# Optimization experiments

Measured on AMD Instinct MI355X. Metric: run time of the kernel, lower is better.

## Reference

```python
import jax, jax.numpy as jnp
import numpy as np
import math

STATE_SIZE = 32


def setup_inputs() -> dict:
    key = jax.random.key(0)
    k1, k2, k3, k4, k5 = jax.random.split(key, 5)
    B, C, H, W = 8, STATE_SIZE, 512, 512
    std = 1.0 / math.sqrt(C)
    states = jax.random.normal(k1, (B, C, H, W), dtype=jnp.float32)
    weight_ih = jax.random.uniform(k2, (3 * C, 3 * C), minval=-std, maxval=std, dtype=jnp.float32)
    bias_ih = jax.random.uniform(k3, (3 * C,), minval=-std, maxval=std, dtype=jnp.float32)
    weight_hh = jax.random.uniform(k4, (3 * C, C), minval=-std, maxval=std, dtype=jnp.float32)
    bias_hh = jax.random.uniform(k5, (3 * C,), minval=-std, maxval=std, dtype=jnp.float32)
    return {"states": states, "weight_ih": weight_ih, "bias_ih": bias_ih,
            "weight_hh": weight_hh, "bias_hh": bias_hh}


def _cell(prev_col, cur_col, weight_ih, bias_ih, weight_hh, bias_hh):
    # prev_col, cur_col: (B, H, C)
    C = cur_col.shape[-1]
    pad = jnp.pad(prev_col, ((0, 0), (1, 1), (0, 0)))  # zero-pad H
    # 3-neighbor gather along H: rows h-1, h, h+1 of previous column
    x = jnp.concatenate([pad[:, :-2], pad[:, 1:-1], pad[:, 2:]], axis=-1)  # (B, H, 3C)
    i_vals = jnp.einsum('bhk,ok->bho', x, weight_ih) + bias_ih            # (B, H, 3C)
    h_vals = jnp.einsum('bhc,oc->bho', cur_col, weight_hh) + bias_hh      # (B, H, 3C)
    r_i, z_i, n_i = jnp.split(i_vals, 3, axis=-1)
    r_h, z_h, n_h = jnp.split(h_vals, 3, axis=-1)
    r = jax.nn.sigmoid(r_i + r_h)
    z = jax.nn.sigmoid(z_i + z_h)
    n = jnp.tanh(n_i + r * n_h)
    return n * z + cur_col * (1.0 - z)


def reference(states, weight_ih, bias_ih, weight_hh, bias_hh):
    # states: (B, C, H, W); scan over W (dir=0, left-to-right)
    s = jnp.transpose(states, (3, 0, 2, 1))  # (W, B, H, C)

    def step(carry, cur_col):
        new_col = _cell(carry, cur_col, weight_ih, bias_ih, weight_hh, bias_hh)
        return new_col, new_col

    col0 = s[0]
    _, cols = jax.lax.scan(step, col0, s[1:])
    out = jnp.concatenate([col0[None], cols], axis=0)  # (W, B, H, C)
    return jnp.transpose(out, (1, 3, 2, 0))  # (B, C, H, W)
```

## Files before the change

kernel.cpp:

```cpp
#include <hip/hip_runtime.h>
#include <stdint.h>
#include <stddef.h>

typedef __attribute__((ext_vector_type(8))) short short8;
typedef __attribute__((ext_vector_type(4))) float floatx4;
typedef unsigned long long u64;

#define Bn 8
#define Cn 32
#define Hn 512
#define Wn 512
#define NCH 32
#define RR 16
#define GR 8
#define WT 8
#define NT (Wn/WT)
#define NWG (Bn*NCH)
#define PST 40
#define OST 9

__device__ __forceinline__ unsigned short f2bf(float f) {
  union { float f; unsigned int i; } v; v.f = f;
  unsigned int x = v.i;
  unsigned int r = x + 0x7fffu + ((x >> 16) & 1u);
  return (unsigned short)(r >> 16);
}
__device__ __forceinline__ float sigmoidf_(float x) {
  return 1.0f / (1.0f + __expf(-x));
}
__device__ __forceinline__ float tanhf_(float x) {
  return 1.0f - 2.0f / (__expf(2.0f * x) + 1.0f);
}

__global__ __launch_bounds__(256, 1) void sdn_scan(
    const float* __restrict__ states,
    const float* __restrict__ wih,
    const float* __restrict__ bih,
    const float* __restrict__ whh,
    const float* __restrict__ bhh,
    float* __restrict__ out,
    u64* __restrict__ bnd)
{
  const int tid = threadIdx.x;
  const int lane = tid & 63;
  const int wid = tid >> 6;
  const int tl = wid >> 1;
  const int tt = wid & 1;
  const int wg = blockIdx.x;
  const int b = wg & 7;
  const int j = wg >> 3;
  const int h0 = j * RR;
  const int lm = lane & 15;
  const int lg = lane >> 4;
  const int cS = lane >> 1;
  const int qS = lane & 1;

  __shared__ __align__(16) unsigned short P[34 * PST];
  __shared__ __align__(16) float INS[WT * 32 * 32];
  __shared__ __align__(16) float OUTS[RR * 32 * OST];

  short8 wf[3][3];
  short8 hf[3];
  float bi[3], bh[3];
  for (int q = 0; q < 3; ++q) {
    const int ot = 2 * q + tt;
    for (int ks = 0; ks < 3; ++ks) {
      short8 v;
#pragma unroll
      for (int t = 0; t < 8; ++t)
        v[t] = (short)f2bf(wih[(size_t)(16 * ot + lm) * 96 + 32 * ks + lg * 8 + t]);
      wf[q][ks] = v;
    }
    short8 v;
#pragma unroll
    for (int t = 0; t < 8; ++t)
      v[t] = (short)f2bf(whh[(size_t)(16 * ot + lm) * 32 + lg * 8 + t]);
    hf[q] = v;
    bi[q] = bih[16 * ot + lm];
    bh[q] = bhh[16 * ot + lm];
  }

  auto stage = [&](int w0) {
    float4 buf[8];
#pragma unroll
    for (int r = 0; r < 8; ++r) {
      int row = 8 * wid + r;
      int h = h0 - GR + row;
      buf[r].x = 0.f; buf[r].y = 0.f; buf[r].z = 0.f; buf[r].w = 0.f;
      if ((unsigned)h < (unsigned)Hn)
        buf[r] = *(const float4*)&states[(((size_t)b * Cn + cS) * Hn + h) * Wn + w0 + 4 * qS];
    }
#pragma unroll
    for (int r = 0; r < 8; ++r) {
      int row = 8 * wid + r;
      float* dst = &INS[row * 32 + cS];
      dst[(4 * qS + 0) * 1024] = buf[r].x;
      dst[(4 * qS + 1) * 1024] = buf[r].y;
      dst[(4 * qS + 2) * 1024] = buf[r].z;
      dst[(4 * qS + 3) * 1024] = buf[r].w;
    }
  };

  stage(0);
  __syncthreads();
  for (int t = tid; t < 34 * 32; t += 256) {
    int pr = t >> 5, c = t & 31;
    int rr = pr - 1;
    unsigned short v = 0;
    if ((unsigned)rr < 32u) v = f2bf(INS[rr * 32 + c]);
    P[pr * PST + c] = v;
  }
  for (int t = tid; t < RR * 32; t += 256) {
    int r = t >> 5, c = t & 31;
    OUTS[(r * 32 + c) * OST + 0] = INS[(r + 8) * 32 + c];
  }
  __syncthreads();

  for (int t = 0; t < NT; ++t) {
    const int w0 = WT * t;

    for (int wi = (t == 0) ? 1 : 0; wi < WT; ++wi) {
      const float* INw = &INS[wi * 1024];

      short8 af[3];
#pragma unroll
      for (int ks = 0; ks < 3; ++ks)
        af[ks] = *(const short8*)&P[(16 * tl + lm + ks) * PST + lg * 8];

      short8 curA;
      {
        const float* ap = &INw[(16 * tl + lm) * 32 + 8 * lg];
#pragma unroll
        for (int u = 0; u < 8; ++u) curA[u] = (short)f2bf(ap[u]);
      }
      float curC[4];
#pragma unroll
      for (int i = 0; i < 4; ++i)
        curC[i] = INw[(16 * tl + 4 * lg + i) * 32 + 16 * tt + lm];

      __syncthreads();

      floatx4 I[3], Hh[3];
#pragma unroll
      for (int q = 0; q < 3; ++q) {
        I[q] = (floatx4){bi[q], bi[q], bi[q], bi[q]};
        Hh[q] = (floatx4){bh[q], bh[q], bh[q], bh[q]};
#pragma unroll
        for (int ks = 0; ks < 3; ++ks)
          I[q] = __builtin_amdgcn_mfma_f32_16x16x32_bf16(af[ks], wf[q][ks], I[q], 0, 0, 0);
        Hh[q] = __builtin_amdgcn_mfma_f32_16x16x32_bf16(curA, hf[q], Hh[q], 0, 0, 0);
      }
#pragma unroll
      for (int i = 0; i < 4; ++i) {
        float rv = sigmoidf_(I[0][i] + Hh[0][i]);
        float zv = sigmoidf_(I[1][i] + Hh[1][i]);
        float nv = tanhf_(I[2][i] + rv * Hh[2][i]);
        float ov = curC[i] + zv * (nv - curC[i]);
        int c = 16 * tt + lm;
        int rr = 16 * tl + 4 * lg + i;
        unsigned short pv = f2bf(ov);
        if ((j == 0 && rr == 7) || (j == NCH - 1 && rr == 24)) pv = 0;
        P[(1 + rr) * PST + c] = pv;
        bool own = (tl == 0) ? (lg >= 2) : (lg < 2);
        if (own)
          OUTS[((rr - 8) * 32 + c) * OST + wi] = ov;
      }

      __syncthreads();
    }

    const int par = t & 1;
    const unsigned int tag = (unsigned int)(w0 + 7);

    if (t < NT - 1) {
      const int dir = tid >> 7;
      const int idx = tid & 127;
      const int row = idx >> 4, cp = (idx & 15) * 2;
      const int prow = (dir ? 17 : 9) + row;
      u64 v = (u64)((unsigned int)P[prow * PST + cp] |
                    ((unsigned int)P[prow * PST + cp + 1] << 16)) | ((u64)tag << 32);
      __hip_atomic_store(&bnd[(size_t)(wg * 2 + par) * 256 + tid], v,
                         __ATOMIC_RELAXED, __HIP_MEMORY_SCOPE_AGENT);
    }

#pragma unroll
    for (int r4 = 0; r4 < 4; ++r4) {
      int r = 4 * wid + r4;
      const float* src = &OUTS[(r * 32 + cS) * OST + 4 * qS];
      float4 v;
      v.x = src[0]; v.y = src[1]; v.z = src[2]; v.w = src[3];
      *(float4*)&out[(((size_t)b * Cn + cS) * Hn + (h0 + r)) * Wn + w0 + 4 * qS] = v;
    }

    if (t < NT - 1) {
      stage(w0 + WT);

      if (tid < 128) {
        if (j > 0) {
          const u64* src = &bnd[(size_t)((wg - 8) * 2 + par) * 256 + 128 + tid];
          u64 v; int spins = 0;
          while (true) {
            v = __hip_atomic_load(src, __ATOMIC_RELAXED, __HIP_MEMORY_SCOPE_AGENT);
            if ((unsigned int)(v >> 32) == tag) break;
            __builtin_amdgcn_s_sleep(2);
            if (++spins > (1 << 20)) break;
          }
          int row = tid >> 4, cp = (tid & 15) * 2;
          P[(1 + row) * PST + cp] = (unsigned short)(v & 0xffffu);
          P[(1 + row) * PST + cp + 1] = (unsigned short)((v >> 16) & 0xffffu);
        }
      } else {
        if (j < NCH - 1) {
          const int idx = tid - 128;
          const u64* src = &bnd[(size_t)((wg + 8) * 2 + par) * 256 + idx];
          u64 v; int spins = 0;
          while (true) {
            v = __hip_atomic_load(src, __ATOMIC_RELAXED, __HIP_MEMORY_SCOPE_AGENT);
            if ((unsigned int)(v >> 32) == tag) break;
            __builtin_amdgcn_s_sleep(2);
            if (++spins > (1 << 20)) break;
          }
          int row = idx >> 4, cp = (idx & 15) * 2;
          P[(25 + row) * PST + cp] = (unsigned short)(v & 0xffffu);
          P[(25 + row) * PST + cp + 1] = (unsigned short)((v >> 16) & 0xffffu);
        }
      }

      __syncthreads();
    }
  }
}

extern "C" void kernel_launch(void* const* d_in, const int* in_sizes, int n_in,
                              void* d_out, int out_size, void* d_ws, size_t ws_size,
                              hipStream_t stream) {
  const float* states = (const float*)d_in[0];
  const float* wih = (const float*)d_in[1];
  const float* bih = (const float*)d_in[2];
  const float* whh = (const float*)d_in[3];
  const float* bhh = (const float*)d_in[4];
  float* outp = (float*)d_out;

  u64* bnd = (u64*)d_ws;

  hipMemsetAsync(bnd, 0, (size_t)NWG * 2 * 256 * sizeof(u64), stream);

  sdn_scan<<<dim3(NWG), dim3(256), 0, stream>>>(states, wih, bih, whh, bhh, outp, bnd);
}
```

Measured before the change: 968.0 us.

## Double-buffer prev column, prefetch next tile, pre-convert bf16 inputs, keep outputs in registers

Double-buffers the bf16 previous-column array so each column step needs one barrier instead of two. The next tile of global input is loaded into registers before the column loop so its latency overlaps compute. Inputs are converted to bf16 once at staging time and the next column's operands are prefetched ahead. Outputs stay in registers and are written straight to global memory, dropping the OUTS shared buffer. In exchange it uses more registers, and the buffer parity logic depends on the tile width being even.

```diff
diff --git a/kernel.cpp b/kernel.cpp
--- a/kernel.cpp
+++ b/kernel.cpp
@@ -17,7 +17,8 @@
 #define NT (Wn/WT)
 #define NWG (Bn*NCH)
 #define PST 40
-#define OST 9
+#define IST 40
+#define IPL (32*IST)
 
 __device__ __forceinline__ unsigned short f2bf(float f) {
   union { float f; unsigned int i; } v; v.f = f;
@@ -55,9 +56,9 @@
   const int cS = lane >> 1;
   const int qS = lane & 1;
 
-  __shared__ __align__(16) unsigned short P[34 * PST];
+  __shared__ __align__(16) unsigned short Pb[2][34 * PST];
   __shared__ __align__(16) float INS[WT * 32 * 32];
-  __shared__ __align__(16) float OUTS[RR * 32 * OST];
+  __shared__ __align__(16) unsigned short INB[WT * IPL];
 
   short8 wf[3][3];
   short8 hf[3];
@@ -80,7 +81,7 @@
     bh[q] = bhh[16 * ot + lm];
   }
 
-  auto stage = [&](int w0) {
+  {
     float4 buf[8];
 #pragma unroll
     for (int r = 0; r < 8; ++r) {
@@ -88,85 +89,119 @@
       int h = h0 - GR + row;
       buf[r].x = 0.f; buf[r].y = 0.f; buf[r].z = 0.f; buf[r].w = 0.f;
       if ((unsigned)h < (unsigned)Hn)
-        buf[r] = *(const float4*)&states[(((size_t)b * Cn + cS) * Hn + h) * Wn + w0 + 4 * qS];
+        buf[r] = *(const float4*)&states[(((size_t)b * Cn + cS) * Hn + h) * Wn + 4 * qS];
     }
 #pragma unroll
     for (int r = 0; r < 8; ++r) {
       int row = 8 * wid + r;
       float* dst = &INS[row * 32 + cS];
-      dst[(4 * qS + 0) * 1024] = buf[r].x;
-      dst[(4 * qS + 1) * 1024] = buf[r].y;
-      dst[(4 * qS + 2) * 1024] = buf[r].z;
-      dst[(4 * qS + 3) * 1024] = buf[r].w;
-    }
-  };
-
-  stage(0);
+      unsigned short* bdst = &INB[row * IST + cS];
+      dst[(4 * qS + 0) * 1024] = buf[r].x;  bdst[(4 * qS + 0) * IPL] = f2bf(buf[r].x);
+      dst[(4 * qS + 1) * 1024] = buf[r].y;  bdst[(4 * qS + 1) * IPL] = f2bf(buf[r].y);
+      dst[(4 * qS + 2) * 1024] = buf[r].z;  bdst[(4 * qS + 2) * IPL] = f2bf(buf[r].z);
+      dst[(4 * qS + 3) * 1024] = buf[r].w;  bdst[(4 * qS + 3) * IPL] = f2bf(buf[r].w);
+    }
+  }
   __syncthreads();
+
   for (int t = tid; t < 34 * 32; t += 256) {
     int pr = t >> 5, c = t & 31;
     int rr = pr - 1;
     unsigned short v = 0;
     if ((unsigned)rr < 32u) v = f2bf(INS[rr * 32 + c]);
-    P[pr * PST + c] = v;
-  }
-  for (int t = tid; t < RR * 32; t += 256) {
-    int r = t >> 5, c = t & 31;
-    OUTS[(r * 32 + c) * OST + 0] = INS[(r + 8) * 32 + c];
+    Pb[0][pr * PST + c] = v;
+  }
+  if (tid < 64) {
+    int pr = (tid >= 32) ? 33 : 0, c = tid & 31;
+    Pb[1][pr * PST + c] = 0;
   }
   __syncthreads();
+
+  float oreg[4][8];
+  {
+    const int c = 16 * tt + lm;
+#pragma unroll
+    for (int i = 0; i < 4; ++i)
+      oreg[i][0] = INS[(16 * tl + 4 * lg + i) * 32 + c];
+  }
+
+  int cur = 0;
 
   for (int t = 0; t < NT; ++t) {
     const int w0 = WT * t;
 
-    for (int wi = (t == 0) ? 1 : 0; wi < WT; ++wi) {
-      const float* INw = &INS[wi * 1024];
+    float4 sbuf[8];
+    if (t < NT - 1) {
+#pragma unroll
+      for (int r = 0; r < 8; ++r) {
+        int row = 8 * wid + r;
+        int h = h0 - GR + row;
+        sbuf[r].x = 0.f; sbuf[r].y = 0.f; sbuf[r].z = 0.f; sbuf[r].w = 0.f;
+        if ((unsigned)h < (unsigned)Hn)
+          sbuf[r] = *(const float4*)&states[(((size_t)b * Cn + cS) * Hn + h) * Wn + (w0 + WT) + 4 * qS];
+      }
+    }
+
+    const int wf0 = (t == 0) ? 1 : 0;
+    short8 curA = *(const short8*)&INB[wf0 * IPL + (16 * tl + lm) * IST + 8 * lg];
+    float curC[4];
+#pragma unroll
+    for (int i = 0; i < 4; ++i)
+      curC[i] = INS[wf0 * 1024 + (16 * tl + 4 * lg + i) * 32 + 16 * tt + lm];
+
+#pragma unroll
+    for (int wi = 0; wi < WT; ++wi) {
+      if (t == 0 && wi == 0) continue;
+      const unsigned short* Pc = Pb[cur];
+      unsigned short* Pn = Pb[cur ^ 1];
 
       short8 af[3];
 #pragma unroll
       for (int ks = 0; ks < 3; ++ks)
-        af[ks] = *(const short8*)&P[(16 * tl + lm + ks) * PST + lg * 8];
-
-      short8 curA;
-      {
-        const float* ap = &INw[(16 * tl + lm) * 32 + 8 * lg];
-#pragma unroll
-        for (int u = 0; u < 8; ++u) curA[u] = (short)f2bf(ap[u]);
-      }
-      float curC[4];
-#pragma unroll
-      for (int i = 0; i < 4; ++i)
-        curC[i] = INw[(16 * tl + 4 * lg + i) * 32 + 16 * tt + lm];
-
-      __syncthreads();
+        af[ks] = *(const short8*)&Pc[(16 * tl + lm + ks) * PST + 8 * lg];
 
       floatx4 I[3], Hh[3];
+#pragma unroll
+      for (int q = 0; q < 3; ++q) {
+        Hh[q] = (floatx4){bh[q], bh[q], bh[q], bh[q]};
+        Hh[q] = __builtin_amdgcn_mfma_f32_16x16x32_bf16(curA, hf[q], Hh[q], 0, 0, 0);
+      }
 #pragma unroll
       for (int q = 0; q < 3; ++q) {
         I[q] = (floatx4){bi[q], bi[q], bi[q], bi[q]};
-        Hh[q] = (floatx4){bh[q], bh[q], bh[q], bh[q]};
 #pragma unroll
         for (int ks = 0; ks < 3; ++ks)
           I[q] = __builtin_amdgcn_mfma_f32_16x16x32_bf16(af[ks], wf[q][ks], I[q], 0, 0, 0);
-        Hh[q] = __builtin_amdgcn_mfma_f32_16x16x32_bf16(curA, hf[q], Hh[q], 0, 0, 0);
-      }
+      }
+
+      short8 nA = curA;
+      float nC[4] = {curC[0], curC[1], curC[2], curC[3]};
+      if (wi < WT - 1) {
+        nA = *(const short8*)&INB[(wi + 1) * IPL + (16 * tl + lm) * IST + 8 * lg];
+#pragma unroll
+        for (int i = 0; i < 4; ++i)
+          nC[i] = INS[(wi + 1) * 1024 + (16 * tl + 4 * lg + i) * 32 + 16 * tt + lm];
+      }
+
+      const int c = 16 * tt + lm;
 #pragma unroll
       for (int i = 0; i < 4; ++i) {
         float rv = sigmoidf_(I[0][i] + Hh[0][i]);
         float zv = sigmoidf_(I[1][i] + Hh[1][i]);
         float nv = tanhf_(I[2][i] + rv * Hh[2][i]);
         float ov = curC[i] + zv * (nv - curC[i]);
-        int c = 16 * tt + lm;
         int rr = 16 * tl + 4 * lg + i;
         unsigned short pv = f2bf(ov);
         if ((j == 0 && rr == 7) || (j == NCH - 1 && rr == 24)) pv = 0;
-        P[(1 + rr) * PST + c] = pv;
-        bool own = (tl == 0) ? (lg >= 2) : (lg < 2);
-        if (own)
-          OUTS[((rr - 8) * 32 + c) * OST + wi] = ov;
+        Pn[(1 + rr) * PST + c] = pv;
+        oreg[i][wi] = ov;
       }
 
       __syncthreads();
+      cur ^= 1;
+      curA = nA;
+#pragma unroll
+      for (int i = 0; i < 4; ++i) curC[i] = nC[i];
     }
 
     const int par = t & 1;
@@ -177,24 +212,42 @@
       const int idx = tid & 127;
       const int row = idx >> 4, cp = (idx & 15) * 2;
       const int prow = (dir ? 17 : 9) + row;
-      u64 v = (u64)((unsigned int)P[prow * PST + cp] |
-                    ((unsigned int)P[prow * PST + cp + 1] << 16)) | ((u64)tag << 32);
+      u64 v = (u64)((unsigned int)Pb[1][prow * PST + cp] |
+                    ((unsigned int)Pb[1][prow * PST + cp + 1] << 16)) | ((u64)tag << 32);
       __hip_atomic_store(&bnd[(size_t)(wg * 2 + par) * 256 + tid], v,
                          __ATOMIC_RELAXED, __HIP_MEMORY_SCOPE_AGENT);
     }
 
-#pragma unroll
-    for (int r4 = 0; r4 < 4; ++r4) {
-      int r = 4 * wid + r4;
-      const float* src = &OUTS[(r * 32 + cS) * OST + 4 * qS];
-      float4 v;
-      v.x = src[0]; v.y = src[1]; v.z = src[2]; v.w = src[3];
-      *(float4*)&out[(((size_t)b * Cn + cS) * Hn + (h0 + r)) * Wn + w0 + 4 * qS] = v;
-    }
-
     if (t < NT - 1) {
-      stage(w0 + WT);
-
+#pragma unroll
+      for (int r = 0; r < 8; ++r) {
+        int row = 8 * wid + r;
+        float* dst = &INS[row * 32 + cS];
+        unsigned short* bdst = &INB[row * IST + cS];
+        dst[(4 * qS + 0) * 1024] = sbuf[r].x;  bdst[(4 * qS + 0) * IPL] = f2bf(sbuf[r].x);
+        dst[(4 * qS + 1) * 1024] = sbuf[r].y;  bdst[(4 * qS + 1) * IPL] = f2bf(sbuf[r].y);
+        dst[(4 * qS + 2) * 1024] = sbuf[r].z;  bdst[(4 * qS + 2) * IPL] = f2bf(sbuf[r].z);
+        dst[(4 * qS + 3) * 1024] = sbuf[r].w;  bdst[(4 * qS + 3) * IPL] = f2bf(sbuf[r].w);
+      }
+    }
+
+    {
+      const bool own = (tl == 0) ? (lg >= 2) : (lg < 2);
+      if (own) {
+        const int c = 16 * tt + lm;
+#pragma unroll
+        for (int i = 0; i < 4; ++i) {
+          int h = h0 + (16 * tl + 4 * lg + i) - 8;
+          float4 lo; lo.x = oreg[i][0]; lo.y = oreg[i][1]; lo.z = oreg[i][2]; lo.w = oreg[i][3];
+          float4 hi; hi.x = oreg[i][4]; hi.y = oreg[i][5]; hi.z = oreg[i][6]; hi.w = oreg[i][7];
+          float* op = &out[(((size_t)b * Cn + c) * Hn + h) * Wn + w0];
+          *(float4*)op = lo;
+          *(float4*)(op + 4) = hi;
+        }
+      }
+    }
+
+    if (t < NT - 1) {
       if (tid < 128) {
         if (j > 0) {
           const u64* src = &bnd[(size_t)((wg - 8) * 2 + par) * 256 + 128 + tid];
@@ -206,8 +259,8 @@
             if (++spins > (1 << 20)) break;
           }
           int row = tid >> 4, cp = (tid & 15) * 2;
-          P[(1 + row) * PST + cp] = (unsigned short)(v & 0xffffu);
-          P[(1 + row) * PST + cp + 1] = (unsigned short)((v >> 16) & 0xffffu);
+          Pb[1][(1 + row) * PST + cp] = (unsigned short)(v & 0xffffu);
+          Pb[1][(1 + row) * PST + cp + 1] = (unsigned short)((v >> 16) & 0xffffu);
         }
       } else {
         if (j < NCH - 1) {
@@ -221,11 +274,10 @@
             if (++spins > (1 << 20)) break;
           }
           int row = idx >> 4, cp = (idx & 15) * 2;
-          P[(25 + row) * PST + cp] = (unsigned short)(v & 0xffffu);
-          P[(25 + row) * PST + cp + 1] = (unsigned short)((v >> 16) & 0xffffu);
+          Pb[1][(25 + row) * PST + cp] = (unsigned short)(v & 0xffffu);
+          Pb[1][(25 + row) * PST + cp + 1] = (unsigned short)((v >> 16) & 0xffffu);
         }
       }
-
       __syncthreads();
     }
   }
```

New measurement: 813.6 us. 1.19x faster.
